# Kernel optimization log

Measured on AMD Instinct MI355X. Metric: run time of the kernel, lower is better.

## Reference

```python
import jax, jax.numpy as jnp
import numpy as np

B, SP, SS = 8, 512, 64          # batch, prefix seq len, suffix seq len
HP, HS = 2048, 1024             # prefix / suffix hidden sizes
NH, NKV, HD = 8, 1, 256         # heads, kv heads, head dim (GQA groups = 8)
IP, IS = 16384, 4096            # MLP intermediate sizes
COND = 1024                     # adaRMSNorm conditioning dim
T = SP + SS
EPS = 1e-6
SCALE = HD ** -0.5
ROPE_BASE = 10000.0


def _rms(x):
    var = jnp.mean(jnp.square(x), axis=-1, keepdims=True)
    return x * jax.lax.rsqrt(var + EPS)


def _rot_half(x):
    x1, x2 = jnp.split(x, 2, axis=-1)
    return jnp.concatenate([-x2, x1], axis=-1)


def setup_inputs() -> dict:
    key = jax.random.key(0)
    ks = iter(jax.random.split(key, 40))
    rn = lambda shape, s=0.02: jax.random.normal(next(ks), shape, dtype=jnp.float32) * s
    return dict(
        x_prefix=rn((B, SP, HP), 1.0),
        x_suffix=rn((B, SS, HS), 1.0),
        cond=rn((B, COND), 1.0),
        attention_mask=jnp.zeros((B, 1, T, T), jnp.float32),
        p_ln1_w=rn((HP,)),
        p_q=rn((NH * HD, HP)), p_k=rn((NKV * HD, HP)), p_v=rn((NKV * HD, HP)), p_o=rn((HP, NH * HD)),
        p_ln2_w=rn((HP,)),
        p_gate=rn((IP, HP)), p_up=rn((IP, HP)), p_down=rn((HP, IP)),
        s_ada1_w=rn((3 * HS, COND)), s_ada1_b=rn((3 * HS,)),
        s_q=rn((NH * HD, HS)), s_k=rn((NKV * HD, HS)), s_v=rn((NKV * HD, HS)), s_o=rn((HS, NH * HD)),
        s_ada2_w=rn((3 * HS, COND)), s_ada2_b=rn((3 * HS,)),
        s_gate=rn((IS, HS)), s_up=rn((IS, HS)), s_down=rn((HS, IS)),
        position_ids=jnp.broadcast_to(jnp.arange(T, dtype=jnp.int32), (B, T)),
    )


def _ada_norm(x, cond, w, b):
    # AdaRMSNormV2: rms(x)*(1+scale)+shift; gate returned separately
    mod = cond @ w.T + b                      # [B, 3*HS]
    scale, shift, gate = jnp.split(mod, 3, axis=-1)
    normed = _rms(x) * (1.0 + scale[:, None, :]) + shift[:, None, :]
    return normed, gate[:, None, :]


def _qkv(h, wq, wk, wv):
    b, t, _ = h.shape
    q = (h @ wq.T).reshape(b, t, NH, HD).transpose(0, 2, 1, 3)   # [B,NH,t,HD]
    k = (h @ wk.T).reshape(b, t, NKV, HD).transpose(0, 2, 1, 3)  # [B,1,t,HD]
    v = (h @ wv.T).reshape(b, t, NKV, HD).transpose(0, 2, 1, 3)
    return q, k, v


def reference(x_prefix, x_suffix, cond, attention_mask,
              p_ln1_w, p_q, p_k, p_v, p_o, p_ln2_w, p_gate, p_up, p_down,
              s_ada1_w, s_ada1_b, s_q, s_k, s_v, s_o, s_ada2_w, s_ada2_b,
              s_gate, s_up, s_down, position_ids):
    # --- pre-attention norms ---
    hp = _rms(x_prefix) * (1.0 + p_ln1_w)                  # plain RMSNorm, gate=None
    hs, gate1 = _ada_norm(x_suffix, cond, s_ada1_w, s_ada1_b)

    qp, kp, vp = _qkv(hp, p_q, p_k, p_v)
    qs, ks, vs = _qkv(hs, s_q, s_k, s_v)
    q = jnp.concatenate([qp, qs], axis=2)                  # [B,NH,T,HD]
    k = jnp.concatenate([kp, ks], axis=2)                  # [B,1,T,HD]
    v = jnp.concatenate([vp, vs], axis=2)

    # --- RoPE over joint sequence ---
    inv_freq = 1.0 / (ROPE_BASE ** (jnp.arange(0, HD, 2, dtype=jnp.float32) / HD))
    freqs = position_ids.astype(jnp.float32)[:, :, None] * inv_freq  # [B,T,HD/2]
    emb = jnp.concatenate([freqs, freqs], axis=-1)
    cos = jnp.cos(emb)[:, None]                            # [B,1,T,HD]
    sin = jnp.sin(emb)[:, None]
    q = q * cos + _rot_half(q) * sin
    k = k * cos + _rot_half(k) * sin

    # --- joint attention (GQA: single kv head broadcast over NH query heads) ---
    k0, v0 = k[:, 0], v[:, 0]                              # [B,T,HD]
    scores = jnp.einsum('bhqd,bkd->bhqk', q, k0) * SCALE
    scores = scores + attention_mask
    probs = jax.nn.softmax(scores, axis=-1)
    attn = jnp.einsum('bhqk,bkd->bhqd', probs, v0)
    attn = attn.transpose(0, 2, 1, 3).reshape(B, T, NH * HD)

    a_p, a_s = attn[:, :SP], attn[:, SP:]

    # --- prefix stream: o_proj + residual + RMSNorm + GeGLU MLP ---
    res_p = x_prefix + a_p @ p_o.T
    h = _rms(res_p) * (1.0 + p_ln2_w)
    mlp_p = (jax.nn.gelu(h @ p_gate.T, approximate=True) * (h @ p_up.T)) @ p_down.T
    out_prefix = res_p + mlp_p

    # --- suffix stream: gated residual + adaRMSNorm + GeGLU MLP + gated residual ---
    res_s = x_suffix + (a_s @ s_o.T) * gate1
    h2, gate2 = _ada_norm(res_s, cond, s_ada2_w, s_ada2_b)
    mlp_s = (jax.nn.gelu(h2 @ s_gate.T, approximate=True) * (h2 @ s_up.T)) @ s_down.T
    out_suffix = res_s + mlp_s * gate2

    return (out_prefix, out_suffix)
```

## Files before the change

kernel.cpp:

```cpp
#include <hip/hip_runtime.h>
#include <cstdint>
#include <cstddef>

typedef __bf16 bf;
typedef __attribute__((ext_vector_type(8))) __bf16 bf16x8;
typedef __attribute__((ext_vector_type(4))) float f32x4;
typedef long long ll;

#define DEV __device__ __forceinline__

constexpr int Tt = 576;
constexpr int NHh = 8;
constexpr float EPSf = 1e-6f;
constexpr float SCALEf = 0.0625f;
constexpr float LN1E4_OVER_128 = 0.07195578515606394f;

constexpr int EPI_F32 = 0, EPI_SCALE_BF16 = 1, EPI_BF16 = 2, EPI_GELU_BF16 = 3,
              EPI_MUL_BF16 = 4, EPI_RES_F32 = 5, EPI_RESGATE_F32 = 6;

DEV float wsum(float v) {
#pragma unroll
  for (int o = 32; o > 0; o >>= 1) v += __shfl_xor(v, o, 64);
  return v;
}
DEV float wmaxr(float v) {
#pragma unroll
  for (int o = 32; o > 0; o >>= 1) v = fmaxf(v, __shfl_xor(v, o, 64));
  return v;
}
DEV float gelu_tanh(float x) {
  float x3 = x * x * x;
  float t = tanhf(0.7978845608028654f * (x + 0.044715f * x3));
  return 0.5f * x * (1.0f + t);
}

DEV void gld16(const void* g, void* l) {
  __builtin_amdgcn_global_load_lds(
      (__attribute__((address_space(1))) void*)(g),
      (__attribute__((address_space(3))) void*)(l), 16, 0, 0);
}


__global__ void f2b_k(const float* __restrict__ s, bf* __restrict__ d, int n8) {
  int i = blockIdx.x * 256 + threadIdx.x;
  int stride = gridDim.x * 256;
  for (; i < n8; i += stride) {
    f32x4 a = ((const f32x4*)s)[i * 2];
    f32x4 b = ((const f32x4*)s)[i * 2 + 1];
    bf16x8 w;
    w[0] = (bf)a[0]; w[1] = (bf)a[1]; w[2] = (bf)a[2]; w[3] = (bf)a[3];
    w[4] = (bf)b[0]; w[5] = (bf)b[1]; w[6] = (bf)b[2]; w[7] = (bf)b[3];
    ((bf16x8*)d)[i] = w;
  }
}

__global__ void rms_scale_2048(const float* __restrict__ x, const float* __restrict__ w,
                               bf* __restrict__ out) {
  int row = blockIdx.x;
  int tid = threadIdx.x;
  const float* xr = x + (ll)row * 2048;
  f32x4 a = *(const f32x4*)(xr + tid * 4);
  f32x4 b = *(const f32x4*)(xr + 1024 + tid * 4);
  float ss = a[0]*a[0]+a[1]*a[1]+a[2]*a[2]+a[3]*a[3]
           + b[0]*b[0]+b[1]*b[1]+b[2]*b[2]+b[3]*b[3];
  ss = wsum(ss);
  __shared__ float red[4];
  if ((tid & 63) == 0) red[tid >> 6] = ss;
  __syncthreads();
  float tot = red[0] + red[1] + red[2] + red[3];
  float sc = rsqrtf(tot * (1.0f / 2048.0f) + EPSf);
  bf* o = out + (ll)row * 2048;
#pragma unroll
  for (int j = 0; j < 4; j++) {
    int c0 = tid * 4 + j;
    o[c0]        = (bf)(a[j] * sc * (1.0f + w[c0]));
    o[1024 + c0] = (bf)(b[j] * sc * (1.0f + w[1024 + c0]));
  }
}

__global__ void ada_mod_k(const float* __restrict__ cond, const float* __restrict__ w,
                          const float* __restrict__ bias, float* __restrict__ mod) {
  int n = blockIdx.x * 256 + threadIdx.x;
  int b = blockIdx.y;
  const float* c = cond + b * 1024;
  const float* wr = w + (ll)n * 1024;
  float s = 0.f;
  for (int k = 0; k < 1024; k += 4) {
    f32x4 cv = *(const f32x4*)(c + k);
    f32x4 wv = *(const f32x4*)(wr + k);
    s += cv[0]*wv[0] + cv[1]*wv[1] + cv[2]*wv[2] + cv[3]*wv[3];
  }
  mod[b * 3072 + n] = s + bias[n];
}

__global__ void ada_norm_k(const float* __restrict__ x, const float* __restrict__ mod,
                           bf* __restrict__ out) {
  int row = blockIdx.x;
  int b = row >> 6;
  int tid = threadIdx.x;
  const float* xr = x + (ll)row * 1024;
  f32x4 a = *(const f32x4*)(xr + tid * 4);
  float ss = a[0]*a[0] + a[1]*a[1] + a[2]*a[2] + a[3]*a[3];
  ss = wsum(ss);
  __shared__ float red[4];
  if ((tid & 63) == 0) red[tid >> 6] = ss;
  __syncthreads();
  float tot = red[0] + red[1] + red[2] + red[3];
  float sc = rsqrtf(tot * (1.0f / 1024.0f) + EPSf);
  const float* m = mod + b * 3072;
  bf* o = out + (ll)row * 1024;
#pragma unroll
  for (int j = 0; j < 4; j++) {
    int c = tid * 4 + j;
    o[c] = (bf)(a[j] * sc * (1.0f + m[c]) + m[1024 + c]);
  }
}

__global__ void rope_k(const float* __restrict__ qbuf, const float* __restrict__ kvbuf,
                       const int* __restrict__ pos, bf* __restrict__ qb,
                       bf* __restrict__ kb, bf* __restrict__ vT) {
  int bt = blockIdx.x;
  int b = bt / Tt, t = bt - b * Tt;
  int tid = threadIdx.x;
  float p = (float)pos[bt];
  const float* qr = qbuf + (ll)bt * 2048;
#pragma unroll
  for (int j = 0; j < 4; j++) {
    int pi = tid + 256 * j;
    int h = pi >> 7, d = pi & 127;
    float ang = p * expf((float)d * (-LN1E4_OVER_128));
    float sn = sinf(ang), cs = cosf(ang);
    float x1 = qr[h * 256 + d], x2 = qr[h * 256 + d + 128];
    bf* qo = qb + ((ll)(b * NHh + h) * Tt + t) * 256;
    qo[d]       = (bf)(x1 * cs - x2 * sn);
    qo[d + 128] = (bf)(x2 * cs + x1 * sn);
  }
  const float* kvr = kvbuf + (ll)bt * 512;
  if (tid < 128) {
    int d = tid;
    float ang = p * expf((float)d * (-LN1E4_OVER_128));
    float sn = sinf(ang), cs = cosf(ang);
    float x1 = kvr[d], x2 = kvr[d + 128];
    bf* ko = kb + (ll)bt * 256;
    ko[d]       = (bf)(x1 * cs - x2 * sn);
    ko[d + 128] = (bf)(x2 * cs + x1 * sn);
  } else {
    int d = tid - 128;
    const float* vv = kvr + 256;
    vT[((ll)b * 256 + d) * Tt + t]       = (bf)vv[d];
    vT[((ll)b * 256 + d + 128) * Tt + t] = (bf)vv[d + 128];
  }
}

__global__ void softmax_k(const bf* __restrict__ scores, const float* __restrict__ mask,
                          bf* __restrict__ probs) {
  int rowg = blockIdx.x * 4 + (threadIdx.x >> 6);
  int lane = threadIdx.x & 63;
  int z = rowg / Tt;
  int t = rowg - z * Tt;
  int b = z >> 3;
  const bf* s = scores + (ll)rowg * Tt;
  const float* mr = mask + ((ll)b * Tt + t) * Tt;
  float v[9];
#pragma unroll
  for (int j = 0; j < 9; j++) {
    int c = lane + j * 64;
    v[j] = (float)s[c] + mr[c];
  }
  float mx = v[0];
#pragma unroll
  for (int j = 1; j < 9; j++) mx = fmaxf(mx, v[j]);
  mx = wmaxr(mx);
  float sum = 0.f;
#pragma unroll
  for (int j = 0; j < 9; j++) { v[j] = __expf(v[j] - mx); sum += v[j]; }
  sum = wsum(sum);
  float inv = 1.0f / sum;
  bf* pr = probs + (ll)rowg * Tt;
#pragma unroll
  for (int j = 0; j < 9; j++) pr[lane + j * 64] = (bf)(v[j] * inv);
}


struct GemmArgs {
  const bf* A; ll sA; int lda;
  const void* Bp; ll sB; int ldb; int zdivB;
  void* C; ll sC; ll sC2; int zdivC; int ldc;
  int M, N, K;
  const float* res; ll sRes;
  const float* gate; ll sGate;
  const bf* aux; ll sAux;
  float alpha;
};

template <int EPI>
DEV void epilogue(const GemmArgs& g, f32x4 (&acc)[4][4], int z, int m0, int n0,
                  int lane, int wr, int wc) {
  const ll coff = (ll)(z / g.zdivC) * g.sC + (ll)(z % g.zdivC) * g.sC2;
  const int r0 = (lane >> 4) * 4;
  const int cc = lane & 15;
#pragma unroll
  for (int m = 0; m < 4; m++) {
#pragma unroll
    for (int n = 0; n < 4; n++) {
      int col = n0 + wc * 64 + n * 16 + cc;
      if (col >= g.N) continue;
#pragma unroll
      for (int r = 0; r < 4; r++) {
        int row = m0 + wr * 64 + m * 16 + r0 + r;
        if (row >= g.M) continue;
        float v = acc[m][n][r];
        ll idx = (ll)row * g.ldc + col;
        if constexpr (EPI == EPI_F32) {
          ((float*)g.C)[coff + idx] = v;
        } else if constexpr (EPI == EPI_SCALE_BF16) {
          ((bf*)g.C)[coff + idx] = (bf)(v * g.alpha);
        } else if constexpr (EPI == EPI_BF16) {
          ((bf*)g.C)[coff + idx] = (bf)v;
        } else if constexpr (EPI == EPI_GELU_BF16) {
          ((bf*)g.C)[coff + idx] = (bf)gelu_tanh(v);
        } else if constexpr (EPI == EPI_MUL_BF16) {
          float a0 = (float)g.aux[(ll)z * g.sAux + idx];
          ((bf*)g.C)[coff + idx] = (bf)(a0 * v);
        } else if constexpr (EPI == EPI_RES_F32) {
          ((float*)g.C)[coff + idx] = g.res[(ll)z * g.sRes + idx] + v;
        } else if constexpr (EPI == EPI_RESGATE_F32) {
          ((float*)g.C)[coff + idx] =
              g.res[(ll)z * g.sRes + idx] + v * g.gate[(ll)z * g.sGate + col];
        }
      }
    }
  }
}

template <int EPI, int BN>
__global__ __launch_bounds__(512) void gemm_8p(GemmArgs g) {
  constexpr int NF = BN / 64;
  constexpr int WN = BN / 4;
  const int z = blockIdx.z;
  const int m0 = blockIdx.x * 256;
  const int n0 = blockIdx.y * BN;
  const int tid = threadIdx.x;
  const int lane = tid & 63;
  const int wv = tid >> 6;
  const int wr = wv >> 2;
  const int wc = wv & 3;

  const bf* A = g.A + (ll)z * g.sA;
  const bf* B = (const bf*)g.Bp + (ll)(z / g.zdivB) * g.sB;

  __shared__ __align__(16) bf lA[2][256 * 64];
  __shared__ __align__(16) bf lB[2][BN * 64];

  f32x4 acc[8][NF];
  f32x4 zero = {0.f, 0.f, 0.f, 0.f};
#pragma unroll
  for (int m = 0; m < 8; m++)
#pragma unroll
    for (int n = 0; n < NF; n++) acc[m][n] = zero;

  const int lrow = lane >> 3;
  const int lsrc = ((lane & 7) ^ lrow) * 8;

  auto stage128 = [&](const bf* src, int ld, int grow0, bf* lds) {
#pragma unroll
    for (int i = 0; i < 2; i++) {
      int chunk = wv * 2 + i;
      gld16(src + (ll)(grow0 + chunk * 8 + lrow) * ld + lsrc, lds + chunk * 512);
    }
  };

  const int NT = g.K >> 6;
  stage128(B, g.ldb, n0, &lB[0][0]);
  if (BN == 256) stage128(B, g.ldb, n0 + 128, &lB[0][128 * 64]);
  stage128(A, g.lda, m0, &lA[0][0]);
  stage128(A, g.lda, m0 + 128, &lA[0][128 * 64]);
  asm volatile("s_waitcnt vmcnt(0)" ::: "memory");
  __builtin_amdgcn_s_barrier();

  for (int t = 0; t < NT; ++t) {
    const int c = t & 1;
    const int nx = (t + 1 < NT) ? t + 1 : t;
    const ll kkn = (ll)nx * 64;
    bf16x8 bv[NF][2];
#pragma unroll
    for (int p = 0; p < 4; ++p) {
      if (p == 0) {
#pragma unroll
        for (int n = 0; n < NF; ++n)
#pragma unroll
          for (int kb = 0; kb < 2; ++kb) {
            int row = wc * WN + n * 16 + (lane & 15);
            int ko = kb * 32 + (lane >> 4) * 8;
            bv[n][kb] = *(const bf16x8*)&lB[c][row * 64 + (ko ^ ((row & 7) * 8))];
          }
      }
      bf16x8 af[2][2];
#pragma unroll
      for (int ml = 0; ml < 2; ++ml)
#pragma unroll
        for (int kb = 0; kb < 2; ++kb) {
          int row = wr * 128 + (2 * p + ml) * 16 + (lane & 15);
          int ko = kb * 32 + (lane >> 4) * 8;
          af[ml][kb] = *(const bf16x8*)&lA[c][row * 64 + (ko ^ ((row & 7) * 8))];
        }
      if (p == 0) {
        stage128(B + kkn, g.ldb, n0, &lB[1 - c][0]);
        if (BN == 256) stage128(B + kkn, g.ldb, n0 + 128, &lB[1 - c][128 * 64]);
      } else if (p == 1) {
        stage128(A + kkn, g.lda, m0, &lA[1 - c][0]);
        stage128(A + kkn, g.lda, m0 + 128, &lA[1 - c][128 * 64]);
      }
      __builtin_amdgcn_s_barrier();
      asm volatile("s_waitcnt lgkmcnt(0)" ::: "memory");
      __builtin_amdgcn_s_setprio(1);
#pragma unroll
      for (int kb = 0; kb < 2; ++kb)
#pragma unroll
        for (int ml = 0; ml < 2; ++ml)
#pragma unroll
          for (int n = 0; n < NF; ++n)
            acc[2 * p + ml][n] = __builtin_amdgcn_mfma_f32_16x16x32_bf16(
                af[ml][kb], bv[n][kb], acc[2 * p + ml][n], 0, 0, 0);
      __builtin_amdgcn_s_setprio(0);
      if (p == 3) asm volatile("s_waitcnt vmcnt(0)" ::: "memory");
      __builtin_amdgcn_s_barrier();
    }
  }

  const ll coff = (ll)(z / g.zdivC) * g.sC + (ll)(z % g.zdivC) * g.sC2;
  const int r0 = (lane >> 4) * 4;
  const int cc = lane & 15;
#pragma unroll
  for (int m = 0; m < 8; m++) {
#pragma unroll
    for (int n = 0; n < NF; n++) {
      int col = n0 + wc * WN + n * 16 + cc;
#pragma unroll
      for (int r = 0; r < 4; r++) {
        int row = m0 + wr * 128 + m * 16 + r0 + r;
        float v = acc[m][n][r];
        ll idx = (ll)row * g.ldc + col;
        if constexpr (EPI == EPI_F32) {
          ((float*)g.C)[coff + idx] = v;
        } else if constexpr (EPI == EPI_GELU_BF16) {
          ((bf*)g.C)[coff + idx] = (bf)gelu_tanh(v);
        } else if constexpr (EPI == EPI_MUL_BF16) {
          float a0 = (float)g.aux[(ll)z * g.sAux + idx];
          ((bf*)g.C)[coff + idx] = (bf)(a0 * v);
        } else if constexpr (EPI == EPI_RES_F32) {
          ((float*)g.C)[coff + idx] = g.res[(ll)z * g.sRes + idx] + v;
        }
      }
    }
  }
}

template <int EPI>
__global__ __launch_bounds__(256) void gemm_p(GemmArgs g) {
  const int z = blockIdx.z;
  const int m0 = blockIdx.x * 128;
  const int n0 = blockIdx.y * 128;
  const int tid = threadIdx.x;
  const int lane = tid & 63;
  const int wid = tid >> 6;
  const int wr = wid >> 1, wc = wid & 1;

  const bf* A = g.A + (ll)z * g.sA;
  const bf* B = (const bf*)g.Bp + (ll)(z / g.zdivB) * g.sB;

  __shared__ __align__(16) bf lA[2][128 * 64];
  __shared__ __align__(16) bf lB[2][128 * 64];

  f32x4 acc[4][4];
  f32x4 zero = {0.f, 0.f, 0.f, 0.f};
#pragma unroll
  for (int m = 0; m < 4; m++)
#pragma unroll
    for (int n = 0; n < 4; n++) acc[m][n] = zero;

  const int lrow = lane >> 3;
  const int lsrc = ((lane & 7) ^ lrow) * 8;

  auto stage = [&](int kt, int bsel) {
    const ll kk = (ll)kt * 64;
#pragma unroll
    for (int i = 0; i < 4; i++) {
      int rr = wid * 32 + i * 8;
      int ra = m0 + rr + lrow; if (ra > g.M - 1) ra = g.M - 1;
      gld16(A + (ll)ra * g.lda + kk + lsrc, &lA[bsel][rr * 64]);
      int rb = n0 + rr + lrow; if (rb > g.N - 1) rb = g.N - 1;
      gld16(B + (ll)rb * g.ldb + kk + lsrc, &lB[bsel][rr * 64]);
    }
  };

  const int nt = g.K >> 6;
  stage(0, 0);
  stage(nt > 1 ? 1 : 0, 1);

  for (int t = 0; t < nt; ++t) {
    const int cur = t & 1;
    asm volatile("s_waitcnt vmcnt(8)" ::: "memory");
    __builtin_amdgcn_s_barrier();
    asm volatile("" ::: "memory");
#pragma unroll
    for (int kb = 0; kb < 2; kb++) {
      const int ko = kb * 32 + (lane >> 4) * 8;
      bf16x8 af[4], bv[4];
#pragma unroll
      for (int m = 0; m < 4; m++) {
        int row = wr * 64 + m * 16 + (lane & 15);
        af[m] = *(const bf16x8*)&lA[cur][row * 64 + (ko ^ ((row & 7) * 8))];
      }
#pragma unroll
      for (int n = 0; n < 4; n++) {
        int row = wc * 64 + n * 16 + (lane & 15);
        bv[n] = *(const bf16x8*)&lB[cur][row * 64 + (ko ^ ((row & 7) * 8))];
      }
      __builtin_amdgcn_s_setprio(1);
#pragma unroll
      for (int m = 0; m < 4; m++)
#pragma unroll
        for (int n = 0; n < 4; n++)
          acc[m][n] = __builtin_amdgcn_mfma_f32_16x16x32_bf16(af[m], bv[n], acc[m][n], 0, 0, 0);
      __builtin_amdgcn_s_setprio(0);
    }
    asm volatile("" ::: "memory");
    __builtin_amdgcn_s_barrier();
    asm volatile("" ::: "memory");
    int nxt = t + 2; if (nxt > nt - 1) nxt = nt - 1;
    stage(nxt, cur);
  }
  epilogue<EPI>(g, acc, z, m0, n0, lane, wr, wc);
}

template <int EPI>
__global__ __launch_bounds__(256) void gemm_rs(GemmArgs g) {
  const int z = blockIdx.z;
  const int m0 = blockIdx.x * 128;
  const int n0 = blockIdx.y * 128;
  const int tid = threadIdx.x;
  const int lane = tid & 63;
  const int wid = tid >> 6;
  const int wr = wid >> 1, wc = wid & 1;

  const bf* A = g.A + (ll)z * g.sA;
  const float* Bf = (const float*)g.Bp + (ll)(z / g.zdivB) * g.sB;

  __shared__ __align__(16) bf lA[128 * 64];
  __shared__ __align__(16) bf lB[128 * 64];

  f32x4 acc[4][4];
  f32x4 zero = {0.f, 0.f, 0.f, 0.f};
#pragma unroll
  for (int m = 0; m < 4; m++)
#pragma unroll
    for (int n = 0; n < 4; n++) acc[m][n] = zero;

  const int srow = tid >> 3;
  const int scol = (tid & 7) * 8;

  for (int kk = 0; kk < g.K; kk += 64) {
#pragma unroll
    for (int i = 0; i < 4; i++) {
      int r = m0 + i * 32 + srow;
      if (r > g.M - 1) r = g.M - 1;
      f32x4 v = *(const f32x4*)(A + (ll)r * g.lda + kk + scol);
      *(f32x4*)&lA[(i * 32 + srow) * 64 + scol] = v;
    }
#pragma unroll
    for (int i = 0; i < 4; i++) {
      int r = n0 + i * 32 + srow;
      if (r > g.N - 1) r = g.N - 1;
      const float* src = Bf + (ll)r * g.ldb + kk + scol;
      f32x4 v0 = *(const f32x4*)(src);
      f32x4 v1 = *(const f32x4*)(src + 4);
      bf16x8 w;
      w[0] = (bf)v0[0]; w[1] = (bf)v0[1]; w[2] = (bf)v0[2]; w[3] = (bf)v0[3];
      w[4] = (bf)v1[0]; w[5] = (bf)v1[1]; w[6] = (bf)v1[2]; w[7] = (bf)v1[3];
      *(bf16x8*)&lB[(i * 32 + srow) * 64 + scol] = w;
    }
    __syncthreads();
#pragma unroll
    for (int kb = 0; kb < 2; kb++) {
      const int ko = kb * 32 + (lane >> 4) * 8;
      bf16x8 af[4], bfv[4];
#pragma unroll
      for (int m = 0; m < 4; m++)
        af[m] = *(const bf16x8*)&lA[(wr * 64 + m * 16 + (lane & 15)) * 64 + ko];
#pragma unroll
      for (int n = 0; n < 4; n++)
        bfv[n] = *(const bf16x8*)&lB[(wc * 64 + n * 16 + (lane & 15)) * 64 + ko];
#pragma unroll
      for (int m = 0; m < 4; m++)
#pragma unroll
        for (int n = 0; n < 4; n++)
          acc[m][n] = __builtin_amdgcn_mfma_f32_16x16x32_bf16(af[m], bfv[n], acc[m][n], 0, 0, 0);
    }
    __syncthreads();
  }
  epilogue<EPI>(g, acc, z, m0, n0, lane, wr, wc);
}


static GemmArgs mkG(const bf* A, ll sA, int lda, const void* Bp, ll sB, int ldb, int zdivB,
                    void* C, ll sC, ll sC2, int zdivC, int ldc, int M, int N, int K) {
  GemmArgs g{};
  g.A = A; g.sA = sA; g.lda = lda;
  g.Bp = Bp; g.sB = sB; g.ldb = ldb; g.zdivB = zdivB;
  g.C = C; g.sC = sC; g.sC2 = sC2; g.zdivC = zdivC; g.ldc = ldc;
  g.M = M; g.N = N; g.K = K;
  g.res = nullptr; g.sRes = 0; g.gate = nullptr; g.sGate = 0; g.aux = nullptr; g.sAux = 0;
  g.alpha = 1.0f;
  return g;
}

extern "C" void kernel_launch(void* const* d_in, const int* in_sizes, int n_in,
                              void* d_out, int out_size, void* d_ws, size_t ws_size,
                              hipStream_t stream) {
  (void)in_sizes; (void)n_in; (void)out_size;
  const float* x_prefix = (const float*)d_in[0];
  const float* x_suffix = (const float*)d_in[1];
  const float* cond     = (const float*)d_in[2];
  const float* mask     = (const float*)d_in[3];
  const float* p_ln1_w  = (const float*)d_in[4];
  const float* p_q      = (const float*)d_in[5];
  const float* p_k      = (const float*)d_in[6];
  const float* p_v      = (const float*)d_in[7];
  const float* p_o      = (const float*)d_in[8];
  const float* p_ln2_w  = (const float*)d_in[9];
  const float* p_gate   = (const float*)d_in[10];
  const float* p_up     = (const float*)d_in[11];
  const float* p_down   = (const float*)d_in[12];
  const float* s_ada1_w = (const float*)d_in[13];
  const float* s_ada1_b = (const float*)d_in[14];
  const float* s_q      = (const float*)d_in[15];
  const float* s_k      = (const float*)d_in[16];
  const float* s_v      = (const float*)d_in[17];
  const float* s_o      = (const float*)d_in[18];
  const float* s_ada2_w = (const float*)d_in[19];
  const float* s_ada2_b = (const float*)d_in[20];
  const float* s_gate   = (const float*)d_in[21];
  const float* s_up     = (const float*)d_in[22];
  const float* s_down   = (const float*)d_in[23];
  const int*   pos      = (const int*)d_in[24];

  char* base = (char*)d_ws;
  size_t off = 0;
  auto alloc = [&](size_t bytes) {
    char* p = base + off;
    off = (off + bytes + 255) & ~(size_t)255;
    return p;
  };
  float* qbuf  = (float*)alloc(8ll * Tt * 2048 * 4);
  float* kvbuf = (float*)alloc(8ll * Tt * 512 * 4);
  bf* hp     = (bf*)alloc(4096ll * 2048 * 2);
  bf* hs     = (bf*)alloc(512ll * 1024 * 2);
  float* mod1 = (float*)alloc(8 * 3072 * 4);
  float* mod2 = (float*)alloc(8 * 3072 * 4);
  bf* qb     = (bf*)alloc(64ll * Tt * 256 * 2);
  bf* kb     = (bf*)alloc(8ll * Tt * 256 * 2);
  bf* vT     = (bf*)alloc(8ll * 256 * Tt * 2);
  bf* scores = (bf*)alloc(64ll * Tt * Tt * 2);
  float* res_p = (float*)alloc(8ll * 512 * 2048 * 4);
  float* res_s = (float*)alloc(8ll * 64 * 1024 * 4);
  bf* gbuf   = (bf*)alloc(4096ll * 16384 * 2);

  bf* attn   = (bf*)qbuf;
  bf* hbuf   = hp;
  bf* h2     = hs;
  bf* probs  = scores;
  bf* gbuf_s = gbuf;

  struct WEnt { const float* src; bf* dst; ll n; };
  WEnt went[14] = {
    {p_q,    nullptr, 2048ll * 2048}, {p_k,    nullptr, 256ll * 2048},
    {p_v,    nullptr, 256ll * 2048},  {p_o,    nullptr, 2048ll * 2048},
    {p_gate, nullptr, 16384ll * 2048},{p_up,   nullptr, 16384ll * 2048},
    {p_down, nullptr, 2048ll * 16384},{s_q,    nullptr, 2048ll * 1024},
    {s_k,    nullptr, 256ll * 1024},  {s_v,    nullptr, 256ll * 1024},
    {s_o,    nullptr, 1024ll * 2048}, {s_gate, nullptr, 4096ll * 1024},
    {s_up,   nullptr, 4096ll * 1024}, {s_down, nullptr, 1024ll * 4096},
  };
  for (int i = 0; i < 14; i++) went[i].dst = (bf*)alloc((size_t)went[i].n * 2);
  const bool conv = (off <= ws_size);

  float* outp = (float*)d_out;
  float* outs = outp + 8ll * 512 * 2048;

  dim3 blk(256);

  if (conv) {
    for (int i = 0; i < 14; i++) {
      int n8 = (int)(went[i].n / 8);
      int grid = (n8 + 255) / 256; if (grid > 4096) grid = 4096;
      f2b_k<<<grid, 256, 0, stream>>>(went[i].src, went[i].dst, n8);
    }
  }
  const bf* w_pq = went[0].dst, *w_pk = went[1].dst, *w_pv = went[2].dst,
          *w_po = went[3].dst, *w_pg = went[4].dst, *w_pu = went[5].dst,
          *w_pd = went[6].dst, *w_sq = went[7].dst, *w_sk = went[8].dst,
          *w_sv = went[9].dst, *w_so = went[10].dst, *w_sg = went[11].dst,
          *w_su = went[12].dst, *w_sd = went[13].dst;

  auto launchW = [&](int epi, GemmArgs g, const float* wf32, const bf* wbf,
                     dim3 grid) {
    if (conv) {
      g.Bp = wbf;
      switch (epi) {
        case EPI_F32:        gemm_p<EPI_F32><<<grid, blk, 0, stream>>>(g); break;
        case EPI_GELU_BF16:  gemm_p<EPI_GELU_BF16><<<grid, blk, 0, stream>>>(g); break;
        case EPI_MUL_BF16:   gemm_p<EPI_MUL_BF16><<<grid, blk, 0, stream>>>(g); break;
        case EPI_RES_F32:    gemm_p<EPI_RES_F32><<<grid, blk, 0, stream>>>(g); break;
        case EPI_RESGATE_F32:gemm_p<EPI_RESGATE_F32><<<grid, blk, 0, stream>>>(g); break;
      }
    } else {
      g.Bp = wf32;
      switch (epi) {
        case EPI_F32:        gemm_rs<EPI_F32><<<grid, blk, 0, stream>>>(g); break;
        case EPI_GELU_BF16:  gemm_rs<EPI_GELU_BF16><<<grid, blk, 0, stream>>>(g); break;
        case EPI_MUL_BF16:   gemm_rs<EPI_MUL_BF16><<<grid, blk, 0, stream>>>(g); break;
        case EPI_RES_F32:    gemm_rs<EPI_RES_F32><<<grid, blk, 0, stream>>>(g); break;
        case EPI_RESGATE_F32:gemm_rs<EPI_RESGATE_F32><<<grid, blk, 0, stream>>>(g); break;
      }
    }
  };

  rms_scale_2048<<<4096, 256, 0, stream>>>(x_prefix, p_ln1_w, hp);
  ada_mod_k<<<dim3(12, 8), 256, 0, stream>>>(cond, s_ada1_w, s_ada1_b, mod1);
  ada_norm_k<<<512, 256, 0, stream>>>(x_suffix, mod1, hs);

  {
    GemmArgs g = mkG(hp, 512ll * 2048, 2048, w_pq, 0, 2048, 1,
                     qbuf, (ll)Tt * 2048, 0, 1, 2048, 512, 2048, 2048);
    if (conv) gemm_8p<EPI_F32, 128><<<dim3(2, 16, 8), 512, 0, stream>>>(g);
    else      launchW(EPI_F32, g, p_q, w_pq, dim3(4, 16, 8));
  }
  launchW(EPI_F32, mkG(hp, 512ll * 2048, 2048, nullptr, 0, 2048, 1,
                       kvbuf, (ll)Tt * 512, 0, 1, 512, 512, 256, 2048),
          p_k, w_pk, dim3(4, 2, 8));
  launchW(EPI_F32, mkG(hp, 512ll * 2048, 2048, nullptr, 0, 2048, 1,
                       kvbuf + 256, (ll)Tt * 512, 0, 1, 512, 512, 256, 2048),
          p_v, w_pv, dim3(4, 2, 8));
  launchW(EPI_F32, mkG(hs, 64ll * 1024, 1024, nullptr, 0, 1024, 1,
                       qbuf + 512ll * 2048, (ll)Tt * 2048, 0, 1, 2048, 64, 2048, 1024),
          s_q, w_sq, dim3(1, 16, 8));
  launchW(EPI_F32, mkG(hs, 64ll * 1024, 1024, nullptr, 0, 1024, 1,
                       kvbuf + 512ll * 512, (ll)Tt * 512, 0, 1, 512, 64, 256, 1024),
          s_k, w_sk, dim3(1, 2, 8));
  launchW(EPI_F32, mkG(hs, 64ll * 1024, 1024, nullptr, 0, 1024, 1,
                       kvbuf + 512ll * 512 + 256, (ll)Tt * 512, 0, 1, 512, 64, 256, 1024),
          s_v, w_sv, dim3(1, 2, 8));
  rope_k<<<8 * Tt, 256, 0, stream>>>(qbuf, kvbuf, pos, qb, kb, vT);

  {
    GemmArgs g = mkG(qb, (ll)Tt * 256, 256, kb, (ll)Tt * 256, 256, 8,
                     scores, (ll)Tt * Tt, 0, 1, Tt, Tt, Tt, 256);
    g.alpha = SCALEf;
    gemm_p<EPI_SCALE_BF16><<<dim3(5, 5, 64), blk, 0, stream>>>(g);
  }
  softmax_k<<<64 * Tt / 4, 256, 0, stream>>>(scores, mask, probs);
  {
    GemmArgs g = mkG(probs, (ll)Tt * Tt, Tt, vT, 256ll * Tt, Tt, 8,
                     attn, (ll)Tt * 2048, 256, 8, 2048, Tt, 256, Tt);
    gemm_p<EPI_BF16><<<dim3(5, 2, 64), blk, 0, stream>>>(g);
  }
  {
    GemmArgs g = mkG(attn, (ll)Tt * 2048, 2048, w_po, 0, 2048, 1,
                     res_p, 512ll * 2048, 0, 1, 2048, 512, 2048, 2048);
    g.res = x_prefix; g.sRes = 512ll * 2048;
    if (conv) gemm_8p<EPI_RES_F32, 128><<<dim3(2, 16, 8), 512, 0, stream>>>(g);
    else      launchW(EPI_RES_F32, g, p_o, w_po, dim3(4, 16, 8));
  }
  {
    GemmArgs g = mkG(attn + 512ll * 2048, (ll)Tt * 2048, 2048, nullptr, 0, 2048, 1,
                     res_s, 64ll * 1024, 0, 1, 1024, 64, 1024, 2048);
    g.res = x_suffix; g.sRes = 64ll * 1024;
    g.gate = mod1 + 2048; g.sGate = 3072;
    launchW(EPI_RESGATE_F32, g, s_o, w_so, dim3(1, 8, 8));
  }
  rms_scale_2048<<<4096, 256, 0, stream>>>(res_p, p_ln2_w, hbuf);
  ada_mod_k<<<dim3(12, 8), 256, 0, stream>>>(cond, s_ada2_w, s_ada2_b, mod2);
  ada_norm_k<<<512, 256, 0, stream>>>(res_s, mod2, h2);

  {
    GemmArgs g = mkG(hbuf, 0, 2048, w_pg, 0, 2048, 1,
                     gbuf, 0, 0, 1, 16384, 4096, 16384, 2048);
    if (conv) gemm_8p<EPI_GELU_BF16, 256><<<dim3(16, 64, 1), 512, 0, stream>>>(g);
    else      launchW(EPI_GELU_BF16, g, p_gate, w_pg, dim3(32, 128, 1));
  }
  {
    GemmArgs g = mkG(hbuf, 0, 2048, w_pu, 0, 2048, 1,
                     gbuf, 0, 0, 1, 16384, 4096, 16384, 2048);
    g.aux = gbuf; g.sAux = 0;
    if (conv) gemm_8p<EPI_MUL_BF16, 256><<<dim3(16, 64, 1), 512, 0, stream>>>(g);
    else      launchW(EPI_MUL_BF16, g, p_up, w_pu, dim3(32, 128, 1));
  }
  {
    GemmArgs g = mkG(gbuf, 0, 16384, w_pd, 0, 16384, 1,
                     outp, 0, 0, 1, 2048, 4096, 2048, 16384);
    g.res = res_p; g.sRes = 0;
    if (conv) gemm_8p<EPI_RES_F32, 128><<<dim3(16, 16, 1), 512, 0, stream>>>(g);
    else      launchW(EPI_RES_F32, g, p_down, w_pd, dim3(32, 16, 1));
  }
  launchW(EPI_GELU_BF16, mkG(h2, 0, 1024, nullptr, 0, 1024, 1,
                             gbuf_s, 0, 0, 1, 4096, 512, 4096, 1024),
          s_gate, w_sg, dim3(4, 32, 1));
  {
    GemmArgs g = mkG(h2, 0, 1024, nullptr, 0, 1024, 1,
                     gbuf_s, 0, 0, 1, 4096, 512, 4096, 1024);
    g.aux = gbuf_s; g.sAux = 0;
    launchW(EPI_MUL_BF16, g, s_up, w_su, dim3(4, 32, 1));
  }
  {
    GemmArgs g = mkG(gbuf_s, 64ll * 4096, 4096, nullptr, 0, 4096, 1,
                     outs, 64ll * 1024, 0, 1, 1024, 64, 1024, 4096);
    g.res = res_s; g.sRes = 64ll * 1024;
    g.gate = mod2 + 2048; g.sGate = 3072;
    launchW(EPI_RESGATE_F32, g, s_down, w_sd, dim3(1, 8, 8));
  }
}
```

Measured before the change: 2.191 ms.

## Triple-buffer the 256x128 GEMM with two-ahead prefetch and XCD-aware block swizzle

```diff
diff --git a/kernel.cpp b/kernel.cpp
--- a/kernel.cpp
+++ b/kernel.cpp
@@ -233,13 +233,16 @@
   }
 }
 
-template <int EPI, int BN>
-__global__ __launch_bounds__(512) void gemm_8p(GemmArgs g) {
-  constexpr int NF = BN / 64;
-  constexpr int WN = BN / 4;
+template <int EPI>
+__global__ __launch_bounds__(512) void gemm_3b(GemmArgs g) {
   const int z = blockIdx.z;
-  const int m0 = blockIdx.x * 256;
-  const int n0 = blockIdx.y * BN;
+  const int nxy = gridDim.x * gridDim.y;
+  const int lin = blockIdx.x + gridDim.x * blockIdx.y;
+  const int q8 = nxy >> 3;
+  const int swz = (lin & 7) * q8 + (lin >> 3);
+  const int m0 = (swz % gridDim.x) * 256;
+  const int n0 = (swz / gridDim.x) * 128;
+
   const int tid = threadIdx.x;
   const int lane = tid & 63;
   const int wv = tid >> 6;
@@ -249,15 +252,15 @@
   const bf* A = g.A + (ll)z * g.sA;
   const bf* B = (const bf*)g.Bp + (ll)(z / g.zdivB) * g.sB;
 
-  __shared__ __align__(16) bf lA[2][256 * 64];
-  __shared__ __align__(16) bf lB[2][BN * 64];
-
-  f32x4 acc[8][NF];
+  __shared__ __align__(16) bf lA[3][256 * 64];
+  __shared__ __align__(16) bf lB[3][128 * 64];
+
+  f32x4 acc[8][2];
   f32x4 zero = {0.f, 0.f, 0.f, 0.f};
 #pragma unroll
   for (int m = 0; m < 8; m++)
 #pragma unroll
-    for (int n = 0; n < NF; n++) acc[m][n] = zero;
+    for (int n = 0; n < 2; n++) acc[m][n] = zero;
 
   const int lrow = lane >> 3;
   const int lsrc = ((lane & 7) ^ lrow) * 8;
@@ -269,31 +272,41 @@
       gld16(src + (ll)(grow0 + chunk * 8 + lrow) * ld + lsrc, lds + chunk * 512);
     }
   };
+  auto stageA = [&](int kt, int b) {
+    const ll kk = (ll)kt * 64;
+    stage128(A + kk, g.lda, m0, &lA[b][0]);
+    stage128(A + kk, g.lda, m0 + 128, &lA[b][128 * 64]);
+  };
+  auto stageB = [&](int kt, int b) {
+    const ll kk = (ll)kt * 64;
+    stage128(B + kk, g.ldb, n0, &lB[b][0]);
+  };
 
   const int NT = g.K >> 6;
-  stage128(B, g.ldb, n0, &lB[0][0]);
-  if (BN == 256) stage128(B, g.ldb, n0 + 128, &lB[0][128 * 64]);
-  stage128(A, g.lda, m0, &lA[0][0]);
-  stage128(A, g.lda, m0 + 128, &lA[0][128 * 64]);
-  asm volatile("s_waitcnt vmcnt(0)" ::: "memory");
+  stageA(0, 0); stageB(0, 0);
+  { int t1 = NT > 1 ? 1 : 0; stageA(t1, 1); stageB(t1, 1); }
+  asm volatile("s_waitcnt vmcnt(6)" ::: "memory");
   __builtin_amdgcn_s_barrier();
 
   for (int t = 0; t < NT; ++t) {
-    const int c = t & 1;
-    const int nx = (t + 1 < NT) ? t + 1 : t;
-    const ll kkn = (ll)nx * 64;
-    bf16x8 bv[NF][2];
+    const int bc = t % 3;
+    const int bn = (t + 2) % 3;
+    const int nx = (t + 2 < NT) ? t + 2 : NT - 1;
+    bf16x8 bv[2][2];
 #pragma unroll
     for (int p = 0; p < 4; ++p) {
       if (p == 0) {
-#pragma unroll
-        for (int n = 0; n < NF; ++n)
+        stageA(nx, bn);
+#pragma unroll
+        for (int n = 0; n < 2; ++n)
 #pragma unroll
           for (int kb = 0; kb < 2; ++kb) {
-            int row = wc * WN + n * 16 + (lane & 15);
+            int row = wc * 32 + n * 16 + (lane & 15);
             int ko = kb * 32 + (lane >> 4) * 8;
-            bv[n][kb] = *(const bf16x8*)&lB[c][row * 64 + (ko ^ ((row & 7) * 8))];
+            bv[n][kb] = *(const bf16x8*)&lB[bc][row * 64 + (ko ^ ((row & 7) * 8))];
           }
+      } else if (p == 1) {
+        stageB(nx, bn);
       }
       bf16x8 af[2][2];
 #pragma unroll
@@ -302,15 +315,8 @@
         for (int kb = 0; kb < 2; ++kb) {
           int row = wr * 128 + (2 * p + ml) * 16 + (lane & 15);
           int ko = kb * 32 + (lane >> 4) * 8;
-          af[ml][kb] = *(const bf16x8*)&lA[c][row * 64 + (ko ^ ((row & 7) * 8))];
+          af[ml][kb] = *(const bf16x8*)&lA[bc][row * 64 + (ko ^ ((row & 7) * 8))];
         }
-      if (p == 0) {
-        stage128(B + kkn, g.ldb, n0, &lB[1 - c][0]);
-        if (BN == 256) stage128(B + kkn, g.ldb, n0 + 128, &lB[1 - c][128 * 64]);
-      } else if (p == 1) {
-        stage128(A + kkn, g.lda, m0, &lA[1 - c][0]);
-        stage128(A + kkn, g.lda, m0 + 128, &lA[1 - c][128 * 64]);
-      }
       __builtin_amdgcn_s_barrier();
       asm volatile("s_waitcnt lgkmcnt(0)" ::: "memory");
       __builtin_amdgcn_s_setprio(1);
@@ -319,11 +325,11 @@
 #pragma unroll
         for (int ml = 0; ml < 2; ++ml)
 #pragma unroll
-          for (int n = 0; n < NF; ++n)
+          for (int n = 0; n < 2; ++n)
             acc[2 * p + ml][n] = __builtin_amdgcn_mfma_f32_16x16x32_bf16(
                 af[ml][kb], bv[n][kb], acc[2 * p + ml][n], 0, 0, 0);
       __builtin_amdgcn_s_setprio(0);
-      if (p == 3) asm volatile("s_waitcnt vmcnt(0)" ::: "memory");
+      if (p == 3) asm volatile("s_waitcnt vmcnt(6)" ::: "memory");
       __builtin_amdgcn_s_barrier();
     }
   }
@@ -334,8 +340,8 @@
 #pragma unroll
   for (int m = 0; m < 8; m++) {
 #pragma unroll
-    for (int n = 0; n < NF; n++) {
-      int col = n0 + wc * WN + n * 16 + cc;
+    for (int n = 0; n < 2; n++) {
+      int col = n0 + wc * 32 + n * 16 + cc;
 #pragma unroll
       for (int r = 0; r < 4; r++) {
         int row = m0 + wr * 128 + m * 16 + r0 + r;
@@ -633,7 +639,7 @@
   {
     GemmArgs g = mkG(hp, 512ll * 2048, 2048, w_pq, 0, 2048, 1,
                      qbuf, (ll)Tt * 2048, 0, 1, 2048, 512, 2048, 2048);
-    if (conv) gemm_8p<EPI_F32, 128><<<dim3(2, 16, 8), 512, 0, stream>>>(g);
+    if (conv) gemm_3b<EPI_F32><<<dim3(2, 16, 8), 512, 0, stream>>>(g);
     else      launchW(EPI_F32, g, p_q, w_pq, dim3(4, 16, 8));
   }
   launchW(EPI_F32, mkG(hp, 512ll * 2048, 2048, nullptr, 0, 2048, 1,
@@ -669,7 +675,7 @@
     GemmArgs g = mkG(attn, (ll)Tt * 2048, 2048, w_po, 0, 2048, 1,
                      res_p, 512ll * 2048, 0, 1, 2048, 512, 2048, 2048);
     g.res = x_prefix; g.sRes = 512ll * 2048;
-    if (conv) gemm_8p<EPI_RES_F32, 128><<<dim3(2, 16, 8), 512, 0, stream>>>(g);
+    if (conv) gemm_3b<EPI_RES_F32><<<dim3(2, 16, 8), 512, 0, stream>>>(g);
     else      launchW(EPI_RES_F32, g, p_o, w_po, dim3(4, 16, 8));
   }
   {
@@ -686,21 +692,21 @@
   {
     GemmArgs g = mkG(hbuf, 0, 2048, w_pg, 0, 2048, 1,
                      gbuf, 0, 0, 1, 16384, 4096, 16384, 2048);
-    if (conv) gemm_8p<EPI_GELU_BF16, 256><<<dim3(16, 64, 1), 512, 0, stream>>>(g);
+    if (conv) gemm_3b<EPI_GELU_BF16><<<dim3(16, 128, 1), 512, 0, stream>>>(g);
     else      launchW(EPI_GELU_BF16, g, p_gate, w_pg, dim3(32, 128, 1));
   }
   {
     GemmArgs g = mkG(hbuf, 0, 2048, w_pu, 0, 2048, 1,
                      gbuf, 0, 0, 1, 16384, 4096, 16384, 2048);
     g.aux = gbuf; g.sAux = 0;
-    if (conv) gemm_8p<EPI_MUL_BF16, 256><<<dim3(16, 64, 1), 512, 0, stream>>>(g);
+    if (conv) gemm_3b<EPI_MUL_BF16><<<dim3(16, 128, 1), 512, 0, stream>>>(g);
     else      launchW(EPI_MUL_BF16, g, p_up, w_pu, dim3(32, 128, 1));
   }
   {
     GemmArgs g = mkG(gbuf, 0, 16384, w_pd, 0, 16384, 1,
                      outp, 0, 0, 1, 2048, 4096, 2048, 16384);
     g.res = res_p; g.sRes = 0;
-    if (conv) gemm_8p<EPI_RES_F32, 128><<<dim3(16, 16, 1), 512, 0, stream>>>(g);
+    if (conv) gemm_3b<EPI_RES_F32><<<dim3(16, 16, 1), 512, 0, stream>>>(g);
     else      launchW(EPI_RES_F32, g, p_down, w_pd, dim3(32, 16, 1));
   }
   launchW(EPI_GELU_BF16, mkG(h2, 0, 1024, nullptr, 0, 1024, 1,
```

Result: slower. 3.019 ms (+37.8%).

## Fuse GeGLU gate and up projections into a single dual-B GEMM kernel

Applied to the files above, without the earlier changes.

```diff
diff --git a/kernel.cpp b/kernel.cpp
--- a/kernel.cpp
+++ b/kernel.cpp
@@ -351,6 +351,124 @@
         } else if constexpr (EPI == EPI_RES_F32) {
           ((float*)g.C)[coff + idx] = g.res[(ll)z * g.sRes + idx] + v;
         }
+      }
+    }
+  }
+}
+
+struct FusedArgs {
+  const bf* A; int lda;
+  const bf* B1; const bf* B2; int ldb;
+  bf* C; int ldc;
+  int K;
+};
+
+__global__ __launch_bounds__(512) void gemm_8pf(FusedArgs g) {
+  const int m0 = blockIdx.x * 256;
+  const int n0 = blockIdx.y * 128;
+  const int tid = threadIdx.x;
+  const int lane = tid & 63;
+  const int wv = tid >> 6;
+  const int wr = wv >> 2;
+  const int wc = wv & 3;
+
+  __shared__ __align__(16) bf lA[2][256 * 64];
+  __shared__ __align__(16) bf lB1[2][128 * 64];
+  __shared__ __align__(16) bf lB2[2][128 * 64];
+
+  f32x4 acc1[8][2], acc2[8][2];
+  f32x4 zero = {0.f, 0.f, 0.f, 0.f};
+#pragma unroll
+  for (int m = 0; m < 8; m++)
+#pragma unroll
+    for (int n = 0; n < 2; n++) { acc1[m][n] = zero; acc2[m][n] = zero; }
+
+  const int lrow = lane >> 3;
+  const int lsrc = ((lane & 7) ^ lrow) * 8;
+
+  auto stage128 = [&](const bf* src, int ld, int grow0, bf* lds) {
+#pragma unroll
+    for (int i = 0; i < 2; i++) {
+      int chunk = wv * 2 + i;
+      gld16(src + (ll)(grow0 + chunk * 8 + lrow) * ld + lsrc, lds + chunk * 512);
+    }
+  };
+
+  const int NT = g.K >> 6;
+  stage128(g.B1, g.ldb, n0, &lB1[0][0]);
+  stage128(g.B2, g.ldb, n0, &lB2[0][0]);
+  stage128(g.A, g.lda, m0, &lA[0][0]);
+  stage128(g.A, g.lda, m0 + 128, &lA[0][128 * 64]);
+  asm volatile("s_waitcnt vmcnt(0)" ::: "memory");
+  __builtin_amdgcn_s_barrier();
+
+  for (int t = 0; t < NT; ++t) {
+    const int c = t & 1;
+    const int nx = (t + 1 < NT) ? t + 1 : t;
+    const ll kkn = (ll)nx * 64;
+    bf16x8 b1v[2][2], b2v[2][2];
+#pragma unroll
+    for (int p = 0; p < 4; ++p) {
+      if (p == 0) {
+#pragma unroll
+        for (int n = 0; n < 2; ++n)
+#pragma unroll
+          for (int kb = 0; kb < 2; ++kb) {
+            int row = wc * 32 + n * 16 + (lane & 15);
+            int ko = kb * 32 + (lane >> 4) * 8;
+            int sw = row * 64 + (ko ^ ((row & 7) * 8));
+            b1v[n][kb] = *(const bf16x8*)&lB1[c][sw];
+            b2v[n][kb] = *(const bf16x8*)&lB2[c][sw];
+          }
+      }
+      bf16x8 af[2][2];
+#pragma unroll
+      for (int ml = 0; ml < 2; ++ml)
+#pragma unroll
+        for (int kb = 0; kb < 2; ++kb) {
+          int row = wr * 128 + (2 * p + ml) * 16 + (lane & 15);
+          int ko = kb * 32 + (lane >> 4) * 8;
+          af[ml][kb] = *(const bf16x8*)&lA[c][row * 64 + (ko ^ ((row & 7) * 8))];
+        }
+      if (p == 0) {
+        stage128(g.B1 + kkn, g.ldb, n0, &lB1[1 - c][0]);
+        stage128(g.B2 + kkn, g.ldb, n0, &lB2[1 - c][0]);
+      } else if (p == 1) {
+        stage128(g.A + kkn, g.lda, m0, &lA[1 - c][0]);
+        stage128(g.A + kkn, g.lda, m0 + 128, &lA[1 - c][128 * 64]);
+      }
+      __builtin_amdgcn_s_barrier();
+      asm volatile("s_waitcnt lgkmcnt(0)" ::: "memory");
+      __builtin_amdgcn_s_setprio(1);
+#pragma unroll
+      for (int kb = 0; kb < 2; ++kb)
+#pragma unroll
+        for (int ml = 0; ml < 2; ++ml)
+#pragma unroll
+          for (int n = 0; n < 2; ++n) {
+            acc1[2 * p + ml][n] = __builtin_amdgcn_mfma_f32_16x16x32_bf16(
+                af[ml][kb], b1v[n][kb], acc1[2 * p + ml][n], 0, 0, 0);
+            acc2[2 * p + ml][n] = __builtin_amdgcn_mfma_f32_16x16x32_bf16(
+                af[ml][kb], b2v[n][kb], acc2[2 * p + ml][n], 0, 0, 0);
+          }
+      __builtin_amdgcn_s_setprio(0);
+      if (p == 3) asm volatile("s_waitcnt vmcnt(0)" ::: "memory");
+      __builtin_amdgcn_s_barrier();
+    }
+  }
+
+  const int r0 = (lane >> 4) * 4;
+  const int cc = lane & 15;
+#pragma unroll
+  for (int m = 0; m < 8; m++) {
+#pragma unroll
+    for (int n = 0; n < 2; n++) {
+      int col = n0 + wc * 32 + n * 16 + cc;
+#pragma unroll
+      for (int r = 0; r < 4; r++) {
+        int row = m0 + wr * 128 + m * 16 + r0 + r;
+        g.C[(ll)row * g.ldc + col] =
+            (bf)(gelu_tanh(acc1[m][n][r]) * acc2[m][n][r]);
       }
     }
   }
@@ -683,18 +801,17 @@
   ada_mod_k<<<dim3(12, 8), 256, 0, stream>>>(cond, s_ada2_w, s_ada2_b, mod2);
   ada_norm_k<<<512, 256, 0, stream>>>(res_s, mod2, h2);
 
-  {
-    GemmArgs g = mkG(hbuf, 0, 2048, w_pg, 0, 2048, 1,
-                     gbuf, 0, 0, 1, 16384, 4096, 16384, 2048);
-    if (conv) gemm_8p<EPI_GELU_BF16, 256><<<dim3(16, 64, 1), 512, 0, stream>>>(g);
-    else      launchW(EPI_GELU_BF16, g, p_gate, w_pg, dim3(32, 128, 1));
-  }
-  {
-    GemmArgs g = mkG(hbuf, 0, 2048, w_pu, 0, 2048, 1,
+  if (conv) {
+    FusedArgs fg{hbuf, 2048, w_pg, w_pu, 2048, gbuf, 16384, 2048};
+    gemm_8pf<<<dim3(16, 128, 1), 512, 0, stream>>>(fg);
+  } else {
+    launchW(EPI_GELU_BF16, mkG(hbuf, 0, 2048, nullptr, 0, 2048, 1,
+                               gbuf, 0, 0, 1, 16384, 4096, 16384, 2048),
+            p_gate, w_pg, dim3(32, 128, 1));
+    GemmArgs g = mkG(hbuf, 0, 2048, nullptr, 0, 2048, 1,
                      gbuf, 0, 0, 1, 16384, 4096, 16384, 2048);
     g.aux = gbuf; g.sAux = 0;
-    if (conv) gemm_8p<EPI_MUL_BF16, 256><<<dim3(16, 64, 1), 512, 0, stream>>>(g);
-    else      launchW(EPI_MUL_BF16, g, p_up, w_pu, dim3(32, 128, 1));
+    launchW(EPI_MUL_BF16, g, p_up, w_pu, dim3(32, 128, 1));
   }
   {
     GemmArgs g = mkG(gbuf, 0, 16384, w_pd, 0, 16384, 1,
@@ -703,10 +820,13 @@
     if (conv) gemm_8p<EPI_RES_F32, 128><<<dim3(16, 16, 1), 512, 0, stream>>>(g);
     else      launchW(EPI_RES_F32, g, p_down, w_pd, dim3(32, 16, 1));
   }
-  launchW(EPI_GELU_BF16, mkG(h2, 0, 1024, nullptr, 0, 1024, 1,
-                             gbuf_s, 0, 0, 1, 4096, 512, 4096, 1024),
-          s_gate, w_sg, dim3(4, 32, 1));
-  {
+  if (conv) {
+    FusedArgs fg{h2, 1024, w_sg, w_su, 1024, gbuf_s, 4096, 1024};
+    gemm_8pf<<<dim3(2, 32, 1), 512, 0, stream>>>(fg);
+  } else {
+    launchW(EPI_GELU_BF16, mkG(h2, 0, 1024, nullptr, 0, 1024, 1,
+                               gbuf_s, 0, 0, 1, 4096, 512, 4096, 1024),
+            s_gate, w_sg, dim3(4, 32, 1));
     GemmArgs g = mkG(h2, 0, 1024, nullptr, 0, 1024, 1,
                      gbuf_s, 0, 0, 1, 4096, 512, 4096, 1024);
     g.aux = gbuf_s; g.sAux = 0;
```

After: 1.944 ms. 11.2% less time.
